# Kernel tuning notes

Hardware: AMD Instinct MI355X
Metric: run time of the kernel (lower is better)

## Reference

```python
import jax, jax.numpy as jnp
import numpy as np

M = 8192          # sketch width
TAU = 64.0
D = 3             # Chebyshev order
SIGMA_DP = 0.01


def setup_inputs() -> dict:
    key = jax.random.key(0)
    ks = jax.random.split(key, 8)
    B, C, K = 512, 4096, 1000
    x = jax.random.normal(ks[0], (B, C), dtype=jnp.float32)
    sketch_mu = jax.random.normal(ks[1], (C, M), dtype=jnp.float32) * 0.1
    g = jnp.where(jax.random.uniform(ks[2], (C,)) < 0.5, -1.0, 1.0).astype(jnp.float32)
    noise = jax.random.normal(ks[3], (C, M), dtype=jnp.float32)
    W = jax.random.normal(ks[4], (C, K), dtype=jnp.float32) * 0.02
    b = jax.random.normal(ks[5], (K,), dtype=jnp.float32) * 0.02
    h = jax.random.randint(ks[6], (C,), 0, M, dtype=jnp.int32)
    t = 10
    return {"x": x, "sketch_mu": sketch_mu, "g": g, "noise": noise,
            "W": W, "b": b, "h": h, "t": t}


def reference(x, sketch_mu, g, noise, W, b, h, t):
    tf = jnp.float32(t)
    lambda_t = 1.0 - jnp.exp(-tf / TAU)
    kappa_t = 1.0 / tf
    # hashed count-sketch scatter-add, vectorized over the batch:
    # per sample i: sketch_mu[:, h] += kappa * (g * x[i])[:, None]
    # under add semantics == kappa * outer(g * sum_i x[i], bincount(h))
    counts = jnp.zeros((M,), dtype=x.dtype).at[h].add(1.0)        # [m]
    update = kappa_t * (g * x.sum(axis=0))[:, None] * counts[None, :]  # [C, m]
    sk = sketch_mu * (1.0 - lambda_t) + update + SIGMA_DP * noise
    # moment estimation
    mu_hat = jnp.mean(sk * g[:, None], axis=1)                    # [C]
    var_hat = jnp.ones_like(mu_hat)
    skew_hat = jnp.zeros_like(mu_hat)
    kurt_hat = jnp.full_like(mu_hat, 3.0)
    # Chebyshev normalization (d = 3 -> all branches active)
    xn = (x - mu_hat) / (jnp.sqrt(var_hat) + 1e-6)
    if D >= 2:
        xn = xn - 0.5 * skew_hat * (xn ** 2 - 1.0)
    if D >= 3:
        xn = xn / jnp.sqrt(kurt_hat / 8.0 + 1e-6)
    # classifier head
    return xn @ W + b
```

## Files before the change

### kernel.cpp

```cpp
#include <hip/hip_runtime.h>
#include <hip/hip_bf16.h>


#define SPLITK 8

typedef float f32x4 __attribute__((ext_vector_type(4)));

__global__ __launch_bounds__(256) void colsum_kernel(const float* __restrict__ x,
                                                     float* __restrict__ colsum,
                                                     int Cdim) {
    int c = blockIdx.x * 256 + threadIdx.x;
    const float* p = x + (size_t)(blockIdx.y * 8) * Cdim + c;
    float r0 = p[0 * (size_t)Cdim];
    float r1 = p[1 * (size_t)Cdim];
    float r2 = p[2 * (size_t)Cdim];
    float r3 = p[3 * (size_t)Cdim];
    float r4 = p[4 * (size_t)Cdim];
    float r5 = p[5 * (size_t)Cdim];
    float r6 = p[6 * (size_t)Cdim];
    float r7 = p[7 * (size_t)Cdim];
    __builtin_amdgcn_sched_barrier(0);
    float acc = ((r0 + r1) + (r2 + r3)) + ((r4 + r5) + (r6 + r7));
    atomicAdd(&colsum[c], acc);
}

__global__ __launch_bounds__(256, 4) void rowsum_kernel(const float* __restrict__ sk,
                                                        const float* __restrict__ noise,
                                                        const float* __restrict__ g,
                                                        const float* __restrict__ colsum,
                                                        const int* __restrict__ t_ptr,
                                                        float* __restrict__ mu,
                                                        int Msk, float hcount) {
    int row = blockIdx.x;
    int tid = threadIdx.x;
    const f32x4* ps = reinterpret_cast<const f32x4*>(sk + (size_t)row * Msk);
    const f32x4* pn = reinterpret_cast<const f32x4*>(noise + (size_t)row * Msk);
    int n4 = Msk >> 2;

    float ss = 0.0f, sn = 0.0f;
    int base = 0;
    for (; base + 2048 <= n4; base += 2048) {
        const f32x4* qs = ps + base + tid;
        const f32x4* qn = pn + base + tid;
        f32x4 a0 = __builtin_nontemporal_load(qs + 0 * 256);
        f32x4 a1 = __builtin_nontemporal_load(qs + 1 * 256);
        f32x4 a2 = __builtin_nontemporal_load(qs + 2 * 256);
        f32x4 a3 = __builtin_nontemporal_load(qs + 3 * 256);
        f32x4 a4 = __builtin_nontemporal_load(qs + 4 * 256);
        f32x4 a5 = __builtin_nontemporal_load(qs + 5 * 256);
        f32x4 a6 = __builtin_nontemporal_load(qs + 6 * 256);
        f32x4 a7 = __builtin_nontemporal_load(qs + 7 * 256);
        f32x4 b0 = __builtin_nontemporal_load(qn + 0 * 256);
        f32x4 b1 = __builtin_nontemporal_load(qn + 1 * 256);
        f32x4 b2 = __builtin_nontemporal_load(qn + 2 * 256);
        f32x4 b3 = __builtin_nontemporal_load(qn + 3 * 256);
        f32x4 b4 = __builtin_nontemporal_load(qn + 4 * 256);
        f32x4 b5 = __builtin_nontemporal_load(qn + 5 * 256);
        f32x4 b6 = __builtin_nontemporal_load(qn + 6 * 256);
        f32x4 b7 = __builtin_nontemporal_load(qn + 7 * 256);
        __builtin_amdgcn_sched_barrier(0);
        float s0 = (a0.x + a0.y) + (a0.z + a0.w);
        float s1 = (a1.x + a1.y) + (a1.z + a1.w);
        float s2 = (a2.x + a2.y) + (a2.z + a2.w);
        float s3 = (a3.x + a3.y) + (a3.z + a3.w);
        float s4 = (a4.x + a4.y) + (a4.z + a4.w);
        float s5 = (a5.x + a5.y) + (a5.z + a5.w);
        float s6 = (a6.x + a6.y) + (a6.z + a6.w);
        float s7 = (a7.x + a7.y) + (a7.z + a7.w);
        float t0 = (b0.x + b0.y) + (b0.z + b0.w);
        float t1 = (b1.x + b1.y) + (b1.z + b1.w);
        float t2 = (b2.x + b2.y) + (b2.z + b2.w);
        float t3 = (b3.x + b3.y) + (b3.z + b3.w);
        float t4 = (b4.x + b4.y) + (b4.z + b4.w);
        float t5 = (b5.x + b5.y) + (b5.z + b5.w);
        float t6 = (b6.x + b6.y) + (b6.z + b6.w);
        float t7 = (b7.x + b7.y) + (b7.z + b7.w);
        ss += ((s0 + s1) + (s2 + s3)) + ((s4 + s5) + (s6 + s7));
        sn += ((t0 + t1) + (t2 + t3)) + ((t4 + t5) + (t6 + t7));
    }
    for (int i = base + tid; i < n4; i += 256) {
        f32x4 v = ps[i];
        f32x4 w = pn[i];
        ss += (v.x + v.y) + (v.z + v.w);
        sn += (w.x + w.y) + (w.z + w.w);
    }

#pragma unroll
    for (int off = 32; off > 0; off >>= 1) {
        ss += __shfl_down(ss, off);
        sn += __shfl_down(sn, off);
    }
    __shared__ float red[2][4];
    int wid = tid >> 6;
    if ((tid & 63) == 0) { red[0][wid] = ss; red[1][wid] = sn; }
    __syncthreads();
    if (tid == 0) {
        float sst = (red[0][0] + red[0][1]) + (red[0][2] + red[0][3]);
        float snt = (red[1][0] + red[1][1]) + (red[1][2] + red[1][3]);
        float t = (float)(*t_ptr);
        float decay = __expf(-t / 64.0f);
        float kappa = 1.0f / t;
        float gc = g[row];
        float acc = decay * sst + 0.01f * snt;
        mu[row] = gc / (float)Msk * (acc + kappa * gc * colsum[row] * hcount);
    }
}

__global__ __launch_bounds__(256) void init_out_kernel(const float* __restrict__ bias,
                                                       float* __restrict__ out,
                                                       int Kdim, int total) {
    int i = blockIdx.x * 256 + threadIdx.x;
    if (i < total) out[i] = bias[i % Kdim];
}

template <bool ATOMIC>
__global__ __launch_bounds__(256, 4) void gemm_kernel(const float* __restrict__ x,
                                                      const float* __restrict__ W,
                                                      const float* __restrict__ mu,
                                                      float* __restrict__ outp,
                                                      int Bdim, int Cdim, int Kdim,
                                                      int cchunk, float s) {
    __shared__ float As[32][68];
    __shared__ float Bs[32][72];

    int row0 = blockIdx.x * 64;
    int col0 = blockIdx.y * 64;
    int cbeg = blockIdx.z * cchunk;

    int tid = threadIdx.x;
    int tx = tid & 15;
    int ty = tid >> 4;
    int a_r = tid >> 2;
    int a_k = (tid & 3) * 4;
    int b_k = tid >> 3;
    int b_c = (tid & 7) * 8;

    float acc[4][4] = {};

    for (int c0 = cbeg; c0 < cbeg + cchunk; c0 += 32) {
        const float* xr = &x[(size_t)(row0 + a_r) * Cdim + c0 + a_k];
        float4 a0 = *reinterpret_cast<const float4*>(xr);
        float4 a1 = *reinterpret_cast<const float4*>(xr + 16);
        float4 m0 = *reinterpret_cast<const float4*>(&mu[c0 + a_k]);
        float4 m1 = *reinterpret_cast<const float4*>(&mu[c0 + a_k + 16]);

        const float* wr = &W[(size_t)(c0 + b_k) * Kdim + col0 + b_c];
        int cb = col0 + b_c;
        float4 b0, b1;
        if (cb + 7 < Kdim) {
            b0 = *reinterpret_cast<const float4*>(wr);
            b1 = *reinterpret_cast<const float4*>(wr + 4);
        } else {
            b0.x = (cb + 0 < Kdim) ? wr[0] : 0.0f;
            b0.y = (cb + 1 < Kdim) ? wr[1] : 0.0f;
            b0.z = (cb + 2 < Kdim) ? wr[2] : 0.0f;
            b0.w = (cb + 3 < Kdim) ? wr[3] : 0.0f;
            b1.x = (cb + 4 < Kdim) ? wr[4] : 0.0f;
            b1.y = (cb + 5 < Kdim) ? wr[5] : 0.0f;
            b1.z = (cb + 6 < Kdim) ? wr[6] : 0.0f;
            b1.w = (cb + 7 < Kdim) ? wr[7] : 0.0f;
        }

        As[a_k + 0][a_r] = s * (a0.x - m0.x);
        As[a_k + 1][a_r] = s * (a0.y - m0.y);
        As[a_k + 2][a_r] = s * (a0.z - m0.z);
        As[a_k + 3][a_r] = s * (a0.w - m0.w);
        As[a_k + 16][a_r] = s * (a1.x - m1.x);
        As[a_k + 17][a_r] = s * (a1.y - m1.y);
        As[a_k + 18][a_r] = s * (a1.z - m1.z);
        As[a_k + 19][a_r] = s * (a1.w - m1.w);
        *reinterpret_cast<float4*>(&Bs[b_k][b_c]) = b0;
        *reinterpret_cast<float4*>(&Bs[b_k][b_c + 4]) = b1;

        __syncthreads();
#pragma unroll
        for (int kk = 0; kk < 32; ++kk) {
            float4 a = *reinterpret_cast<const float4*>(&As[kk][ty * 4]);
            float4 b = *reinterpret_cast<const float4*>(&Bs[kk][tx * 4]);
            acc[0][0] += a.x * b.x; acc[0][1] += a.x * b.y;
            acc[0][2] += a.x * b.z; acc[0][3] += a.x * b.w;
            acc[1][0] += a.y * b.x; acc[1][1] += a.y * b.y;
            acc[1][2] += a.y * b.z; acc[1][3] += a.y * b.w;
            acc[2][0] += a.z * b.x; acc[2][1] += a.z * b.y;
            acc[2][2] += a.z * b.z; acc[2][3] += a.z * b.w;
            acc[3][0] += a.w * b.x; acc[3][1] += a.w * b.y;
            acc[3][2] += a.w * b.z; acc[3][3] += a.w * b.w;
        }
        __syncthreads();
    }

#pragma unroll
    for (int j = 0; j < 4; ++j) {
        int row = row0 + ty * 4 + j;
        int col = col0 + tx * 4;
        if (ATOMIC) {
#pragma unroll
            for (int l = 0; l < 4; ++l)
                if (col + l < Kdim)
                    atomicAdd(&outp[(size_t)row * Kdim + col + l], acc[j][l]);
        } else {
            float* pp = &outp[((size_t)blockIdx.z * Bdim + row) * Kdim + col];
            if (col + 3 < Kdim) {
                float4 v;
                v.x = acc[j][0]; v.y = acc[j][1]; v.z = acc[j][2]; v.w = acc[j][3];
                *reinterpret_cast<float4*>(pp) = v;
            } else {
#pragma unroll
                for (int l = 0; l < 4; ++l)
                    if (col + l < Kdim) pp[l] = acc[j][l];
            }
        }
    }
}

__global__ __launch_bounds__(256) void reduce_kernel(const float* __restrict__ part,
                                                     const float* __restrict__ bias,
                                                     float* __restrict__ out,
                                                     int total4, int Kdim, int perz) {
    int i = blockIdx.x * 256 + threadIdx.x;
    if (i >= total4) return;
    const float4* p4 = reinterpret_cast<const float4*>(part);
    float4 sum = p4[i];
#pragma unroll
    for (int z = 1; z < SPLITK; ++z) {
        float4 v = p4[(size_t)z * (perz >> 2) + i];
        sum.x += v.x; sum.y += v.y; sum.z += v.z; sum.w += v.w;
    }
    int e = i * 4;
    sum.x += bias[(e + 0) % Kdim];
    sum.y += bias[(e + 1) % Kdim];
    sum.z += bias[(e + 2) % Kdim];
    sum.w += bias[(e + 3) % Kdim];
    reinterpret_cast<float4*>(out)[i] = sum;
}

extern "C" void kernel_launch(void* const* d_in, const int* in_sizes, int n_in,
                              void* d_out, int out_size, void* d_ws, size_t ws_size,
                              hipStream_t stream) {
    const float* x      = (const float*)d_in[0];
    const float* sk     = (const float*)d_in[1];
    const float* g      = (const float*)d_in[2];
    const float* noise  = (const float*)d_in[3];
    const float* W      = (const float*)d_in[4];
    const float* bias   = (const float*)d_in[5];
    const int* t_ptr    = (const int*)d_in[7];

    int C    = in_sizes[2];
    int Bdim = in_sizes[0] / C;
    int Msk  = in_sizes[1] / C;
    int Kdim = in_sizes[5];
    float hcount = (float)in_sizes[6];

    float* colsum = (float*)d_ws;
    float* mu     = colsum + C;
    float* part   = mu + C;

    size_t need = (size_t)(2 * C + SPLITK * Bdim * Kdim) * sizeof(float);
    bool use_partial = ws_size >= need;

    float s = (float)(1.0 / ((1.0 + 1e-6) * sqrt(0.375 + 1e-6)));
    int cchunk = C / SPLITK;

    hipMemsetAsync(colsum, 0, C * sizeof(float), stream);
    {
        dim3 grid(C / 256, Bdim / 8);
        colsum_kernel<<<grid, 256, 0, stream>>>(x, colsum, C);
    }
    rowsum_kernel<<<C, 256, 0, stream>>>(sk, noise, g, colsum, t_ptr, mu, Msk, hcount);
    dim3 ggrid(Bdim / 64, (Kdim + 63) / 64, SPLITK);
    if (use_partial) {
        gemm_kernel<false><<<ggrid, 256, 0, stream>>>(x, W, mu, part, Bdim, C, Kdim,
                                                      cchunk, s);
        int perz = Bdim * Kdim;
        int total4 = perz / 4;
        reduce_kernel<<<(total4 + 255) / 256, 256, 0, stream>>>(part, bias,
                                                                (float*)d_out,
                                                                total4, Kdim, perz);
    } else {
        int total = Bdim * Kdim;
        init_out_kernel<<<(total + 255) / 256, 256, 0, stream>>>(bias, (float*)d_out,
                                                                 Kdim, total);
        gemm_kernel<true><<<ggrid, 256, 0, stream>>>(x, W, mu, (float*)d_out, Bdim, C,
                                                     Kdim, cchunk, s);
    }
}
```

Baseline: 341.9 us.

## Use bf16x3 split MFMA for the normalized classifier GEMM

Replaces the scalar FMA tiled GEMM with MFMA 16x16x32 bf16 instructions. Each fp32 operand is split into high and low bf16 parts, and three MFMA products are summed to keep near-fp32 accuracy. The aim is to cut the fp32 ALU cost of the GEMM, at the price of conversion work, extra shared-memory traffic, and scalar W loads and output stores.

```diff
diff --git a/kernel.cpp b/kernel.cpp
--- a/kernel.cpp
+++ b/kernel.cpp
@@ -5,6 +5,16 @@
 #define SPLITK 8
 
 typedef float f32x4 __attribute__((ext_vector_type(4)));
+typedef short bf16x8 __attribute__((ext_vector_type(8)));
+
+__device__ __forceinline__ short f2bf(float f) {
+    unsigned u = __float_as_uint(f);
+    unsigned r = (u + 0x7FFFu + ((u >> 16) & 1u)) >> 16;
+    return (short)r;
+}
+__device__ __forceinline__ float bf2f(short b) {
+    return __uint_as_float(((unsigned)(unsigned short)b) << 16);
+}
 
 __global__ __launch_bounds__(256) void colsum_kernel(const float* __restrict__ x,
                                                      float* __restrict__ colsum,
@@ -119,95 +129,113 @@
                                                       const float* __restrict__ mu,
                                                       float* __restrict__ outp,
                                                       int Bdim, int Cdim, int Kdim,
-                                                      int cchunk, float s) {
-    __shared__ float As[32][68];
-    __shared__ float Bs[32][72];
-
-    int row0 = blockIdx.x * 64;
-    int col0 = blockIdx.y * 64;
-    int cbeg = blockIdx.z * cchunk;
-
-    int tid = threadIdx.x;
-    int tx = tid & 15;
-    int ty = tid >> 4;
-    int a_r = tid >> 2;
-    int a_k = (tid & 3) * 4;
-    int b_k = tid >> 3;
-    int b_c = (tid & 7) * 8;
-
-    float acc[4][4] = {};
-
-    for (int c0 = cbeg; c0 < cbeg + cchunk; c0 += 32) {
-        const float* xr = &x[(size_t)(row0 + a_r) * Cdim + c0 + a_k];
-        float4 a0 = *reinterpret_cast<const float4*>(xr);
-        float4 a1 = *reinterpret_cast<const float4*>(xr + 16);
-        float4 m0 = *reinterpret_cast<const float4*>(&mu[c0 + a_k]);
-        float4 m1 = *reinterpret_cast<const float4*>(&mu[c0 + a_k + 16]);
-
-        const float* wr = &W[(size_t)(c0 + b_k) * Kdim + col0 + b_c];
-        int cb = col0 + b_c;
-        float4 b0, b1;
-        if (cb + 7 < Kdim) {
-            b0 = *reinterpret_cast<const float4*>(wr);
-            b1 = *reinterpret_cast<const float4*>(wr + 4);
-        } else {
-            b0.x = (cb + 0 < Kdim) ? wr[0] : 0.0f;
-            b0.y = (cb + 1 < Kdim) ? wr[1] : 0.0f;
-            b0.z = (cb + 2 < Kdim) ? wr[2] : 0.0f;
-            b0.w = (cb + 3 < Kdim) ? wr[3] : 0.0f;
-            b1.x = (cb + 4 < Kdim) ? wr[4] : 0.0f;
-            b1.y = (cb + 5 < Kdim) ? wr[5] : 0.0f;
-            b1.z = (cb + 6 < Kdim) ? wr[6] : 0.0f;
-            b1.w = (cb + 7 < Kdim) ? wr[7] : 0.0f;
-        }
-
-        As[a_k + 0][a_r] = s * (a0.x - m0.x);
-        As[a_k + 1][a_r] = s * (a0.y - m0.y);
-        As[a_k + 2][a_r] = s * (a0.z - m0.z);
-        As[a_k + 3][a_r] = s * (a0.w - m0.w);
-        As[a_k + 16][a_r] = s * (a1.x - m1.x);
-        As[a_k + 17][a_r] = s * (a1.y - m1.y);
-        As[a_k + 18][a_r] = s * (a1.z - m1.z);
-        As[a_k + 19][a_r] = s * (a1.w - m1.w);
-        *reinterpret_cast<float4*>(&Bs[b_k][b_c]) = b0;
-        *reinterpret_cast<float4*>(&Bs[b_k][b_c + 4]) = b1;
+                                                      int Kc, float s) {
+    __shared__ short As[2][64][40];
+    __shared__ short Bs[2][64][40];
+
+    const int tid = threadIdx.x;
+    const int lane = tid & 63;
+    const int w = tid >> 6;
+    const int wr = w >> 1;
+    const int wc = w & 1;
+    const int row0 = blockIdx.x * 64;
+    const int col0 = blockIdx.y * 64;
+    const int cbeg = blockIdx.z * Kc;
+
+    const int am = tid >> 2;
+    const int ac8 = (tid & 3) * 8;
+    const int bn = tid & 63;
+    const int bk8 = (tid >> 6) * 8;
+    const int bcol = col0 + bn;
+    const bool bok = bcol < Kdim;
+
+    const int fr = lane & 15;
+    const int fk8 = (lane >> 4) * 8;
+
+    f32x4 acc[2][2] = {};
+
+    for (int it = 0; it < Kc; it += 32) {
+        const int c0 = cbeg + it;
+        const float* xr = &x[(size_t)(row0 + am) * Cdim + c0 + ac8];
+        f32x4 xa = *reinterpret_cast<const f32x4*>(xr);
+        f32x4 xb = *reinterpret_cast<const f32x4*>(xr + 4);
+        f32x4 ma = *reinterpret_cast<const f32x4*>(&mu[c0 + ac8]);
+        f32x4 mb = *reinterpret_cast<const f32x4*>(&mu[c0 + ac8 + 4]);
+        float wv[8];
+#pragma unroll
+        for (int j = 0; j < 8; ++j)
+            wv[j] = bok ? W[(size_t)(c0 + bk8 + j) * Kdim + bcol] : 0.0f;
 
         __syncthreads();
-#pragma unroll
-        for (int kk = 0; kk < 32; ++kk) {
-            float4 a = *reinterpret_cast<const float4*>(&As[kk][ty * 4]);
-            float4 b = *reinterpret_cast<const float4*>(&Bs[kk][tx * 4]);
-            acc[0][0] += a.x * b.x; acc[0][1] += a.x * b.y;
-            acc[0][2] += a.x * b.z; acc[0][3] += a.x * b.w;
-            acc[1][0] += a.y * b.x; acc[1][1] += a.y * b.y;
-            acc[1][2] += a.y * b.z; acc[1][3] += a.y * b.w;
-            acc[2][0] += a.z * b.x; acc[2][1] += a.z * b.y;
-            acc[2][2] += a.z * b.z; acc[2][3] += a.z * b.w;
-            acc[3][0] += a.w * b.x; acc[3][1] += a.w * b.y;
-            acc[3][2] += a.w * b.z; acc[3][3] += a.w * b.w;
-        }
+
+        float av[8];
+        av[0] = s * (xa.x - ma.x); av[1] = s * (xa.y - ma.y);
+        av[2] = s * (xa.z - ma.z); av[3] = s * (xa.w - ma.w);
+        av[4] = s * (xb.x - mb.x); av[5] = s * (xb.y - mb.y);
+        av[6] = s * (xb.z - mb.z); av[7] = s * (xb.w - mb.w);
+        bf16x8 ah, al;
+#pragma unroll
+        for (int j = 0; j < 8; ++j) {
+            short h = f2bf(av[j]);
+            ah[j] = h;
+            al[j] = f2bf(av[j] - bf2f(h));
+        }
+        *reinterpret_cast<bf16x8*>(&As[0][am][ac8]) = ah;
+        *reinterpret_cast<bf16x8*>(&As[1][am][ac8]) = al;
+
+        bf16x8 bh, bl;
+#pragma unroll
+        for (int j = 0; j < 8; ++j) {
+            short h = f2bf(wv[j]);
+            bh[j] = h;
+            bl[j] = f2bf(wv[j] - bf2f(h));
+        }
+        *reinterpret_cast<bf16x8*>(&Bs[0][bn][bk8]) = bh;
+        *reinterpret_cast<bf16x8*>(&Bs[1][bn][bk8]) = bl;
+
         __syncthreads();
-    }
-
-#pragma unroll
-    for (int j = 0; j < 4; ++j) {
-        int row = row0 + ty * 4 + j;
-        int col = col0 + tx * 4;
-        if (ATOMIC) {
-#pragma unroll
-            for (int l = 0; l < 4; ++l)
-                if (col + l < Kdim)
-                    atomicAdd(&outp[(size_t)row * Kdim + col + l], acc[j][l]);
-        } else {
-            float* pp = &outp[((size_t)blockIdx.z * Bdim + row) * Kdim + col];
-            if (col + 3 < Kdim) {
-                float4 v;
-                v.x = acc[j][0]; v.y = acc[j][1]; v.z = acc[j][2]; v.w = acc[j][3];
-                *reinterpret_cast<float4*>(pp) = v;
-            } else {
-#pragma unroll
-                for (int l = 0; l < 4; ++l)
-                    if (col + l < Kdim) pp[l] = acc[j][l];
+
+        bf16x8 afr[2][2], bfr[2][2];
+#pragma unroll
+        for (int h = 0; h < 2; ++h) {
+#pragma unroll
+            for (int f = 0; f < 2; ++f) {
+                afr[h][f] = *reinterpret_cast<const bf16x8*>(
+                    &As[h][wr * 32 + f * 16 + fr][fk8]);
+                bfr[h][f] = *reinterpret_cast<const bf16x8*>(
+                    &Bs[h][wc * 32 + f * 16 + fr][fk8]);
+            }
+        }
+
+#pragma unroll
+        for (int mf = 0; mf < 2; ++mf) {
+#pragma unroll
+            for (int nf = 0; nf < 2; ++nf) {
+                acc[mf][nf] = __builtin_amdgcn_mfma_f32_16x16x32_bf16(
+                    afr[0][mf], bfr[0][nf], acc[mf][nf], 0, 0, 0);
+                acc[mf][nf] = __builtin_amdgcn_mfma_f32_16x16x32_bf16(
+                    afr[0][mf], bfr[1][nf], acc[mf][nf], 0, 0, 0);
+                acc[mf][nf] = __builtin_amdgcn_mfma_f32_16x16x32_bf16(
+                    afr[1][mf], bfr[0][nf], acc[mf][nf], 0, 0, 0);
+            }
+        }
+    }
+
+#pragma unroll
+    for (int mf = 0; mf < 2; ++mf) {
+#pragma unroll
+        for (int nf = 0; nf < 2; ++nf) {
+#pragma unroll
+            for (int r = 0; r < 4; ++r) {
+                int row = row0 + wr * 32 + mf * 16 + (lane >> 4) * 4 + r;
+                int col = col0 + wc * 32 + nf * 16 + (lane & 15);
+                if (col < Kdim) {
+                    if (ATOMIC)
+                        atomicAdd(&outp[(size_t)row * Kdim + col], acc[mf][nf][r]);
+                    else
+                        outp[((size_t)blockIdx.z * Bdim + row) * Kdim + col] =
+                            acc[mf][nf][r];
+                }
             }
         }
     }
@@ -259,7 +287,7 @@
     bool use_partial = ws_size >= need;
 
     float s = (float)(1.0 / ((1.0 + 1e-6) * sqrt(0.375 + 1e-6)));
-    int cchunk = C / SPLITK;
+    int Kc = C / SPLITK;
 
     hipMemsetAsync(colsum, 0, C * sizeof(float), stream);
     {
@@ -270,7 +298,7 @@
     dim3 ggrid(Bdim / 64, (Kdim + 63) / 64, SPLITK);
     if (use_partial) {
         gemm_kernel<false><<<ggrid, 256, 0, stream>>>(x, W, mu, part, Bdim, C, Kdim,
-                                                      cchunk, s);
+                                                      Kc, s);
         int perz = Bdim * Kdim;
         int total4 = perz / 4;
         reduce_kernel<<<(total4 + 255) / 256, 256, 0, stream>>>(part, bias,
@@ -281,6 +309,6 @@
         init_out_kernel<<<(total + 255) / 256, 256, 0, stream>>>(bias, (float*)d_out,
                                                                  Kdim, total);
         gemm_kernel<true><<<ggrid, 256, 0, stream>>>(x, W, mu, (float*)d_out, Bdim, C,
-                                                     Kdim, cchunk, s);
-    }
-}
+                                                     Kdim, Kc, s);
+    }
+}
```

Measured after the change: 313.3 us. 8.3% less time.
